# Kernel optimization log

Measured on AMD Instinct MI355X. Metric: run time of the kernel, lower is better.

The kernel has to match this reference:

```python
import jax, jax.numpy as jnp
import numpy as np

B, S, D, H = 2, 2048, 1024, 16
HD = D // H  # 64


def setup_inputs() -> dict:
    key = jax.random.key(0)
    k1, k2, k3, k4, k5, k6 = jax.random.split(key, 6)
    x = jax.random.normal(k1, (B, S, D), dtype=jnp.float32)
    # binary mask source (1.0 = masked-out position), multiplied by -1e9 inside
    mask = (jax.random.uniform(k2, (B, S, S), dtype=jnp.float32) < 0.1).astype(jnp.float32)
    lim = 1.0 / np.sqrt(D)
    Wqkv = jax.random.uniform(k3, (D, 3 * D), dtype=jnp.float32, minval=-lim, maxval=lim)
    bqkv = jax.random.uniform(k4, (3 * D,), dtype=jnp.float32, minval=-lim, maxval=lim)
    Wo = jax.random.uniform(k5, (D, D), dtype=jnp.float32, minval=-lim, maxval=lim)
    bo = jax.random.uniform(k6, (D,), dtype=jnp.float32, minval=-lim, maxval=lim)
    return {"x": x, "mask": mask, "Wqkv": Wqkv, "bqkv": bqkv, "Wo": Wo, "bo": bo}


def reference(x, mask, Wqkv, bqkv, Wo, bo):
    b, s, d = x.shape
    qkv = x @ Wqkv + bqkv                              # [B,S,3D]
    qkv = qkv.reshape(b, s, 3, H, HD).transpose(2, 0, 3, 1, 4)  # [3,B,H,S,HD]
    q, k, v = qkv[0], qkv[1], qkv[2]
    scale = 1.0 / jnp.sqrt(jnp.float32(HD))
    scores = jnp.einsum('bhqd,bhkd->bhqk', q, k) * scale
    scores = scores + mask[:, None, :, :] * (-1e9)     # broadcast over heads
    attn = jax.nn.softmax(scores, axis=-1)             # [B,H,S,S]
    values = jnp.einsum('bhqk,bhkd->bhqd', attn, v)    # [B,H,S,HD]
    # faithful to source: permute(1,0,2,3) then reshape(B,S,H*HD)
    values = values.transpose(1, 0, 2, 3).reshape(b, s, H * HD)
    return values @ Wo + bo
```

## Files before the change

### kernel.cpp

```cpp
#include <hip/hip_runtime.h>
#include <stdint.h>

#define BB 2
#define SS 2048
#define DD 1024
#define HH 16
#define HD 64
#define BH 32
#define BS 4096

typedef short bf16x8 __attribute__((ext_vector_type(8)));
typedef float f32x4 __attribute__((ext_vector_type(4)));

static __device__ __forceinline__ unsigned short f2bf(float f) {
    union { float f; unsigned int u; } x;
    x.f = f;
    unsigned int u = x.u;
    unsigned int r = u + 0x7FFFu + ((u >> 16) & 1u);
    return (unsigned short)(r >> 16);
}

static __device__ __forceinline__ void gld16(unsigned short* lds, const unsigned short* g) {
    __builtin_amdgcn_global_load_lds(
        (const __attribute__((address_space(1))) unsigned int*)g,
        (__attribute__((address_space(3))) unsigned int*)lds,
        16, 0, 0);
}

__global__ __launch_bounds__(256) void prep(
    const float* __restrict__ x, unsigned short* __restrict__ xb,
    const float* __restrict__ Wqkv, unsigned short* __restrict__ WqkvT,
    const float* __restrict__ Wo, unsigned short* __restrict__ WoT,
    const float* __restrict__ mask, unsigned int* __restrict__ mbitsT) {
    __shared__ float tile[32][33];
    int bid = blockIdx.x;
    int tid = threadIdx.x;
    if (bid < 4096) {
        int i = (bid * 256 + tid) * 4;
        float4 v = *(const float4*)(x + i);
        ushort4 o;
        o.x = f2bf(v.x); o.y = f2bf(v.y); o.z = f2bf(v.z); o.w = f2bf(v.w);
        *(ushort4*)(xb + i) = o;
    } else if (bid < 8192) {
        const float* W;
        unsigned short* WT;
        int N, t;
        if (bid < 7168) { W = Wqkv; WT = WqkvT; N = 3072; t = bid - 4096; }
        else            { W = Wo;   WT = WoT;   N = 1024; t = bid - 7168; }
        const int K = 1024;
        int nx = N >> 5;
        int n0 = (t % nx) * 32, k0 = (t / nx) * 32;
        int tx = tid & 31, ty = tid >> 5;
#pragma unroll
        for (int i = 0; i < 4; i++)
            tile[ty + i * 8][tx] = W[(size_t)(k0 + ty + i * 8) * N + n0 + tx];
        __syncthreads();
#pragma unroll
        for (int i = 0; i < 4; i++)
            WT[(size_t)(n0 + ty + i * 8) * K + k0 + tx] = f2bf(tile[tx][ty + i * 8]);
    } else {
        size_t i = (size_t)(bid - 8192) * 256 + tid;
        float v = mask[i];
        unsigned long long bal = __ballot(v != 0.0f);
        int lane = tid & 63;
        int kw = (int)((i & 2047) >> 5);
        int sq = (int)((i >> 11) & 2047);
        int b = (int)(i >> 22);
        if (lane == 0)
            mbitsT[((size_t)b * 64 + kw) * 2048 + sq] = (unsigned int)bal;
        else if (lane == 32)
            mbitsT[((size_t)b * 64 + kw) * 2048 + sq] = (unsigned int)(bal >> 32);
    }
}

__global__ __launch_bounds__(256) void qkv_gemm(
    const unsigned short* __restrict__ xb,
    const unsigned short* __restrict__ WqkvT,
    const float* __restrict__ bqkv,
    unsigned short* __restrict__ q_ws,
    unsigned short* __restrict__ k_ws,
    unsigned short* __restrict__ vB) {
    __shared__ unsigned short ldsA[4096], ldsB[4096];
    int gx = blockIdx.x;
    int tid = threadIdx.x;
    int m0 = (gx / 24) * 128, n0 = (gx % 24) * 128;
    int w = tid >> 6, lane = tid & 63, quad = lane >> 4, l15 = lane & 15;

    int r = tid >> 2, p = tid & 3;
    int c = (p - (r >> 1)) & 3;
    const unsigned short* gA0 = xb + (size_t)(m0 + r) * 1024 + c * 8;
    const unsigned short* gA1 = gA0 + (size_t)64 * 1024;
    const unsigned short* gB0 = WqkvT + (size_t)(n0 + r) * 1024 + c * 8;
    const unsigned short* gB1 = gB0 + (size_t)64 * 1024;
    unsigned short* lA0 = ldsA + w * 512;
    unsigned short* lA1 = ldsA + 2048 + w * 512;
    unsigned short* lB0 = ldsB + w * 512;
    unsigned short* lB1 = ldsB + 2048 + w * 512;

    int wm = w >> 1, wn = w & 1;
    int posq = ((quad + (l15 >> 1)) & 3) * 8;
    int aoff = (wm * 64 + l15) * 32 + posq;
    int boff = (wn * 64 + l15) * 32 + posq;

    f32x4 acc[4][4] = {};
    for (int k0 = 0; k0 < 1024; k0 += 32) {
        __syncthreads();
        gld16(lA0, gA0 + k0);
        gld16(lA1, gA1 + k0);
        gld16(lB0, gB0 + k0);
        gld16(lB1, gB1 + k0);
        __syncthreads();
        bf16x8 af[4], bfr[4];
#pragma unroll
        for (int i = 0; i < 4; i++) {
            af[i]  = *(const bf16x8*)(ldsA + aoff + i * 512);
            bfr[i] = *(const bf16x8*)(ldsB + boff + i * 512);
        }
#pragma unroll
        for (int i = 0; i < 4; i++)
#pragma unroll
            for (int j = 0; j < 4; j++)
                acc[i][j] = __builtin_amdgcn_mfma_f32_16x16x32_bf16(af[i], bfr[j], acc[i][j], 0, 0, 0);
    }

    int t = n0 >> 10;
    int ncol0 = n0 + wn * 64;
    int hh = (ncol0 >> 6) & 15;
    int Rb = m0 + wm * 64 + quad * 4;

    if (t == 2) {
        int rowbase = m0 + wm * 64;
        int b = rowbase >> 11;
        int kt = (rowbase >> 6) & 31;
        int bh = b * 16 + hh;
#pragma unroll
        for (int j = 0; j < 4; j++) {
            int hd = j * 16 + l15;
            float bias = bqkv[ncol0 + hd];
#pragma unroll
            for (int i = 0; i < 4; i++) {
                unsigned short* dst = vB +
                    (((((size_t)bh * 32 + kt) * 2 + (i >> 1)) * 4 + quad) * 64 + hd) * 8 + (i & 1) * 4;
                ushort4 pk;
                pk.x = f2bf(acc[i][j][0] + bias);
                pk.y = f2bf(acc[i][j][1] + bias);
                pk.z = f2bf(acc[i][j][2] + bias);
                pk.w = f2bf(acc[i][j][3] + bias);
                *(ushort4*)dst = pk;
            }
        }
    } else {
        unsigned short* dst = (t == 0) ? q_ws : k_ws;
#pragma unroll
        for (int j = 0; j < 4; j++) {
            int hd = j * 16 + l15;
            float bias = bqkv[ncol0 + hd];
#pragma unroll
            for (int i = 0; i < 4; i++) {
                int row = Rb + i * 16;
                int b = row >> 11, s = row & 2047;
                int bh = b * 16 + hh;
#pragma unroll
                for (int rr = 0; rr < 4; rr++)
                    dst[((size_t)(bh * 2048 + s + rr)) * 64 + hd] = f2bf(acc[i][j][rr] + bias);
            }
        }
    }
}

__global__ __launch_bounds__(256) void out_gemm(
    const unsigned short* __restrict__ Amat,
    const unsigned short* __restrict__ WoT,
    const float* __restrict__ bo,
    float* __restrict__ out) {
    __shared__ unsigned short ldsA[4096], ldsB[2048];
    int gx = blockIdx.x;
    int m0 = (gx / 16) * 128, n0 = (gx % 16) * 64;
    int tid = threadIdx.x;
    int w = tid >> 6, lane = tid & 63, quad = lane >> 4, l15 = lane & 15;

    int r = tid >> 2, p = tid & 3;
    int c = (p - (r >> 1)) & 3;
    const unsigned short* gA0 = Amat + (size_t)(m0 + r) * 1024 + c * 8;
    const unsigned short* gA1 = gA0 + (size_t)64 * 1024;
    const unsigned short* gB0 = WoT + (size_t)(n0 + r) * 1024 + c * 8;
    unsigned short* lA0 = ldsA + w * 512;
    unsigned short* lA1 = ldsA + 2048 + w * 512;
    unsigned short* lB0 = ldsB + w * 512;

    int wm = w >> 1, wn = w & 1;
    int posq = ((quad + (l15 >> 1)) & 3) * 8;
    int aoff = (wm * 64 + l15) * 32 + posq;
    int boff = (wn * 32 + l15) * 32 + posq;

    f32x4 acc[4][2] = {};
    for (int k0 = 0; k0 < 1024; k0 += 32) {
        __syncthreads();
        gld16(lA0, gA0 + k0);
        gld16(lA1, gA1 + k0);
        gld16(lB0, gB0 + k0);
        __syncthreads();
        bf16x8 af[4], bfr[2];
#pragma unroll
        for (int i = 0; i < 4; i++) af[i] = *(const bf16x8*)(ldsA + aoff + i * 512);
#pragma unroll
        for (int j = 0; j < 2; j++) bfr[j] = *(const bf16x8*)(ldsB + boff + j * 512);
#pragma unroll
        for (int i = 0; i < 4; i++)
#pragma unroll
            for (int j = 0; j < 2; j++)
                acc[i][j] = __builtin_amdgcn_mfma_f32_16x16x32_bf16(af[i], bfr[j], acc[i][j], 0, 0, 0);
    }
    int ncol0 = n0 + wn * 32;
    int Rb = m0 + wm * 64 + quad * 4;
#pragma unroll
    for (int j = 0; j < 2; j++) {
        int col = ncol0 + j * 16 + l15;
        float bias = bo[col];
#pragma unroll
        for (int i = 0; i < 4; i++) {
            int row = Rb + i * 16;
#pragma unroll
            for (int rr = 0; rr < 4; rr++)
                out[(size_t)(row + rr) * 1024 + col] = acc[i][j][rr] + bias;
        }
    }
}

__global__ __launch_bounds__(256) void attn(
    const unsigned short* __restrict__ q_ws,
    const unsigned short* __restrict__ k_ws,
    const unsigned short* __restrict__ vB,
    const unsigned int* __restrict__ mbitsT,
    unsigned short* __restrict__ o_ws) {
    __shared__ unsigned short ldsK[8192];
    __shared__ unsigned short ldsV[8192];

    int tid = threadIdx.x;
    int w = tid >> 6, lane = tid & 63, quad = lane >> 4, l15 = lane & 15;
    int bxr = blockIdx.x;
    int bx = ((bxr & 7) << 7) | (bxr >> 3);
    int bh = bx >> 5, qt = bx & 31;
    int b = bh >> 4, h = bh & 15;

    int q = qt * 64 + w * 16 + l15;
    const unsigned short* qptr = q_ws + ((size_t)(bh * 2048 + q)) * 64 + quad * 8;
    bf16x8 qf0 = *(const bf16x8*)(qptr);
    bf16x8 qf1 = *(const bf16x8*)(qptr + 32);

    const float c2 = 0.125f * 1.44269504089f;
    const float Cs = c2 * 8388608.0f;
    const float Ds = (127.0f - 16.0f) * 8388608.0f;

    const unsigned int* mb = mbitsT + (size_t)b * 64 * 2048 + q;
    const unsigned short* kbase = k_ws + (size_t)bh * 2048 * 64;
    const unsigned short* vbb = vB + (size_t)bh * 32 * 4096;

    int srow = (lane >> 3);
    int spos = lane & 7;
    unsigned short* dK0 = ldsK + w * 1024 + lane * 8;
    unsigned short* dV0 = ldsV + w * 1024 + lane * 8;
    int r0 = w * 16 + srow;
    int r1 = r0 + 8;
    int g0 = spos ^ (r0 & 7);
    int g1 = spos ^ (r1 & 7);
    const unsigned short* kS0n = kbase + (size_t)r0 * 64 + g0 * 8;
    const unsigned short* kS1n = kbase + (size_t)r1 * 64 + g1 * 8;
    const unsigned short* vSn  = vbb + (size_t)w * 1024 + lane * 8;
    const unsigned int* mbn = mb;

    f32x4 oacc[4] = {};
    f32x4 lacc = {};
    bf16x8 onesA;
#pragma unroll
    for (int j = 0; j < 8; j++) onesA[j] = (short)0x3F80;

    int sw = (l15 & 7);
    int q4 = quad * 4;

    gld16(dK0, kS0n);
    gld16(dK0 + 512, kS1n);
    gld16(dV0, vSn);
    gld16(dV0 + 512, vSn + 512);
    kS0n += 4096; kS1n += 4096; vSn += 4096;
    unsigned int mw0 = mbn[0];
    unsigned int mw1 = mbn[2048];
    mbn += 4096;
    __syncthreads();

    unsigned int nw0, nw1;

#define ATTN_BODY(KT, CO)                                                          \
    {                                                                              \
        nw0 = 0; nw1 = 0;                                                          \
        if ((KT) < 31) {                 \
            gld16(dK0 + ((CO) ^ 4096), kS0n);                                      \
            gld16(dK0 + ((CO) ^ 4096) + 512, kS1n);                                \
            gld16(dV0 + ((CO) ^ 4096), vSn);                                       \
            gld16(dV0 + ((CO) ^ 4096) + 512, vSn + 512);                           \
            kS0n += 4096; kS1n += 4096; vSn += 4096;                               \
            nw0 = mbn[0]; nw1 = mbn[2048]; mbn += 4096;                            \
        }                                                                          \
        f32x4 sacc[4];                                                             \
        __builtin_amdgcn_s_setprio(1);                                             \
        _Pragma("unroll")                                                          \
        for (int nt = 0; nt < 4; nt++) {                                           \
            const unsigned short* kr = ldsK + (CO) + (nt * 16 + l15) * 64;         \
            bf16x8 kf0, kf1;                                                       \
            __builtin_memcpy(&kf0, kr + (quad ^ sw) * 8, 16);                      \
            __builtin_memcpy(&kf1, kr + ((quad + 4) ^ sw) * 8, 16);                \
            f32x4 z = {};                                                          \
            z = __builtin_amdgcn_mfma_f32_16x16x32_bf16(kf0, qf0, z, 0, 0, 0);     \
            z = __builtin_amdgcn_mfma_f32_16x16x32_bf16(kf1, qf1, z, 0, 0, 0);     \
            sacc[nt] = z;                                                          \
        }                                                                          \
        __builtin_amdgcn_s_setprio(0);                                             \
        unsigned int s0 = mw0 >> q4;                                               \
        unsigned int s1 = mw1 >> q4;                                               \
        unsigned int dw[4][2];                                                     \
        _Pragma("unroll")                                                          \
        for (int nt = 0; nt < 4; nt++) {                                           \
            unsigned int sel = (nt & 2) ? s1 : s0;                                 \
            unsigned int u[4];                                                     \
            _Pragma("unroll")                                                      \
            for (int rr = 0; rr < 4; rr++) {                                       \
                float y = __builtin_fmaf(sacc[nt][rr], Cs, Ds);                    \
                if ((sel >> ((nt & 1) * 16 + rr)) & 1u) y = 0.f;                   \
                u[rr] = (unsigned int)(int)y;                                      \
            }                                                                      \
            dw[nt][0] = __builtin_amdgcn_perm(u[1], u[0], 0x07060302u);            \
            dw[nt][1] = __builtin_amdgcn_perm(u[3], u[2], 0x07060302u);            \
        }                                                                          \
        __builtin_amdgcn_s_setprio(1);                                             \
        _Pragma("unroll")                                                          \
        for (int ks2 = 0; ks2 < 2; ks2++) {                                        \
            union { bf16x8 v; unsigned int d[4]; } bfr;                            \
            bfr.d[0] = dw[2 * ks2][0];                                             \
            bfr.d[1] = dw[2 * ks2][1];                                             \
            bfr.d[2] = dw[2 * ks2 + 1][0];                                         \
            bfr.d[3] = dw[2 * ks2 + 1][1];                                         \
            _Pragma("unroll")                                                      \
            for (int nb = 0; nb < 4; nb++) {                                       \
                bf16x8 vf;                                                         \
                __builtin_memcpy(&vf,                                              \
                    ldsV + (CO) + ((ks2 * 4 + quad) * 64 + nb * 16 + l15) * 8, 16);\
                oacc[nb] = __builtin_amdgcn_mfma_f32_16x16x32_bf16(vf, bfr.v,      \
                                                                   oacc[nb], 0, 0, 0); \
            }                                                                      \
            lacc = __builtin_amdgcn_mfma_f32_16x16x32_bf16(onesA, bfr.v, lacc,     \
                                                           0, 0, 0);               \
        }                                                                          \
        __builtin_amdgcn_s_setprio(0);                                             \
        __syncthreads();               \
        mw0 = nw0; mw1 = nw1;                                                      \
    }

    for (int kt = 0; kt < 32; kt += 2) {
        ATTN_BODY(kt, 0);
        ATTN_BODY(kt + 1, 4096);
    }
#undef ATTN_BODY

    float linv = 1.0f / lacc[0];
    unsigned short* base = o_ws + ((size_t)((h * 2 + b) * 2048 + q)) * 64;
#pragma unroll
    for (int nb = 0; nb < 4; nb++) {
        ushort4 pk;
        pk.x = f2bf(oacc[nb][0] * linv);
        pk.y = f2bf(oacc[nb][1] * linv);
        pk.z = f2bf(oacc[nb][2] * linv);
        pk.w = f2bf(oacc[nb][3] * linv);
        *(ushort4*)(base + nb * 16 + quad * 4) = pk;
    }
}


extern "C" void kernel_launch(void* const* d_in, const int* in_sizes, int n_in,
                              void* d_out, int out_size, void* d_ws, size_t ws_size,
                              hipStream_t stream) {
    const float* x    = (const float*)d_in[0];
    const float* mask = (const float*)d_in[1];
    const float* Wqkv = (const float*)d_in[2];
    const float* bqkv = (const float*)d_in[3];
    const float* Wo   = (const float*)d_in[4];
    const float* bo   = (const float*)d_in[5];
    float* out = (float*)d_out;

    char* ws = (char*)d_ws;
    unsigned short* xb    = (unsigned short*)(ws);
    unsigned short* WqkvT = (unsigned short*)(ws + ((size_t)8 << 20));
    unsigned short* WoT   = (unsigned short*)(ws + ((size_t)14 << 20));
    unsigned short* q_ws  = (unsigned short*)(ws + ((size_t)16 << 20));
    unsigned short* k_ws  = (unsigned short*)(ws + ((size_t)24 << 20));
    unsigned short* vB    = (unsigned short*)(ws + ((size_t)32 << 20));
    unsigned short* o_ws  = (unsigned short*)(ws + ((size_t)40 << 20));
    unsigned int*   mbits = (unsigned int*)(ws + ((size_t)48 << 20));

    prep<<<8192 + 32768, 256, 0, stream>>>(x, xb, Wqkv, WqkvT, Wo, WoT, mask, mbits);
    qkv_gemm<<<768, 256, 0, stream>>>(xb, WqkvT, bqkv, q_ws, k_ws, vB);
    attn<<<1024, 256, 0, stream>>>(q_ws, k_ws, vB, mbits, o_ws);
    out_gemm<<<512, 256, 0, stream>>>(o_ws, WoT, bo, out);
}
```

Measured before the change: 232.3 us.

## Split attention waves across key halves with two query tiles each, reduce via LDS

Each of the four waves in the attention block now handles 32 queries (two 16-query tiles) over half of each 64-key tile, instead of 16 queries over the full key tile. Every K fragment read from LDS and every V fragment is now reused for two MFMA query tiles, roughly halving LDS fragment reads per MFMA. The two key-half partial output and row-sum accumulators are merged through LDS at the end. This costs an extra barrier and reduction, plus more accumulator registers per thread.

```diff
diff --git a/kernel.cpp b/kernel.cpp
--- a/kernel.cpp
+++ b/kernel.cpp
@@ -238,21 +238,25 @@
 
     int tid = threadIdx.x;
     int w = tid >> 6, lane = tid & 63, quad = lane >> 4, l15 = lane & 15;
+    int wk = w >> 1, wq = w & 1;
     int bxr = blockIdx.x;
     int bx = ((bxr & 7) << 7) | (bxr >> 3);
     int bh = bx >> 5, qt = bx & 31;
     int b = bh >> 4, h = bh & 15;
 
-    int q = qt * 64 + w * 16 + l15;
-    const unsigned short* qptr = q_ws + ((size_t)(bh * 2048 + q)) * 64 + quad * 8;
-    bf16x8 qf0 = *(const bf16x8*)(qptr);
-    bf16x8 qf1 = *(const bf16x8*)(qptr + 32);
+    int qA = qt * 64 + wq * 32 + l15;
+    const unsigned short* qptrA = q_ws + ((size_t)(bh * 2048 + qA)) * 64 + quad * 8;
+    bf16x8 qfA0 = *(const bf16x8*)(qptrA);
+    bf16x8 qfA1 = *(const bf16x8*)(qptrA + 32);
+    const unsigned short* qptrB = qptrA + 16 * 64;
+    bf16x8 qfB0 = *(const bf16x8*)(qptrB);
+    bf16x8 qfB1 = *(const bf16x8*)(qptrB + 32);
 
     const float c2 = 0.125f * 1.44269504089f;
     const float Cs = c2 * 8388608.0f;
     const float Ds = (127.0f - 16.0f) * 8388608.0f;
 
-    const unsigned int* mb = mbitsT + (size_t)b * 64 * 2048 + q;
+    const unsigned int* mbn = mbitsT + (size_t)b * 64 * 2048 + qA + (size_t)wk * 2048;
     const unsigned short* kbase = k_ws + (size_t)bh * 2048 * 64;
     const unsigned short* vbb = vB + (size_t)bh * 32 * 4096;
 
@@ -267,92 +271,99 @@
     const unsigned short* kS0n = kbase + (size_t)r0 * 64 + g0 * 8;
     const unsigned short* kS1n = kbase + (size_t)r1 * 64 + g1 * 8;
     const unsigned short* vSn  = vbb + (size_t)w * 1024 + lane * 8;
-    const unsigned int* mbn = mb;
-
-    f32x4 oacc[4] = {};
-    f32x4 lacc = {};
+
+    f32x4 oaccA[4] = {}, oaccB[4] = {};
+    f32x4 laccA = {}, laccB = {};
     bf16x8 onesA;
 #pragma unroll
     for (int j = 0; j < 8; j++) onesA[j] = (short)0x3F80;
 
     int sw = (l15 & 7);
     int q4 = quad * 4;
+    int krow = wk * 32;
+    int voff = (wk * 4 + quad) * 64;
 
     gld16(dK0, kS0n);
     gld16(dK0 + 512, kS1n);
     gld16(dV0, vSn);
     gld16(dV0 + 512, vSn + 512);
     kS0n += 4096; kS1n += 4096; vSn += 4096;
-    unsigned int mw0 = mbn[0];
-    unsigned int mw1 = mbn[2048];
+    unsigned int mwA = mbn[0];
+    unsigned int mwB = mbn[16];
     mbn += 4096;
     __syncthreads();
 
-    unsigned int nw0, nw1;
+    unsigned int nwA, nwB;
 
 #define ATTN_BODY(KT, CO)                                                          \
     {                                                                              \
-        nw0 = 0; nw1 = 0;                                                          \
+        nwA = 0; nwB = 0;                                                          \
         if ((KT) < 31) {                 \
             gld16(dK0 + ((CO) ^ 4096), kS0n);                                      \
             gld16(dK0 + ((CO) ^ 4096) + 512, kS1n);                                \
             gld16(dV0 + ((CO) ^ 4096), vSn);                                       \
             gld16(dV0 + ((CO) ^ 4096) + 512, vSn + 512);                           \
             kS0n += 4096; kS1n += 4096; vSn += 4096;                               \
-            nw0 = mbn[0]; nw1 = mbn[2048]; mbn += 4096;                            \
+            nwA = mbn[0]; nwB = mbn[16]; mbn += 4096;                              \
         }                                                                          \
-        f32x4 sacc[4];                                                             \
+        f32x4 saccA[2], saccB[2];                                                  \
         __builtin_amdgcn_s_setprio(1);                                             \
         _Pragma("unroll")                                                          \
-        for (int nt = 0; nt < 4; nt++) {                                           \
-            const unsigned short* kr = ldsK + (CO) + (nt * 16 + l15) * 64;         \
+        for (int i = 0; i < 2; i++) {                                              \
+            const unsigned short* kr = ldsK + (CO) + (krow + i * 16 + l15) * 64;   \
             bf16x8 kf0, kf1;                                                       \
             __builtin_memcpy(&kf0, kr + (quad ^ sw) * 8, 16);                      \
             __builtin_memcpy(&kf1, kr + ((quad + 4) ^ sw) * 8, 16);                \
-            f32x4 z = {};                                                          \
-            z = __builtin_amdgcn_mfma_f32_16x16x32_bf16(kf0, qf0, z, 0, 0, 0);     \
-            z = __builtin_amdgcn_mfma_f32_16x16x32_bf16(kf1, qf1, z, 0, 0, 0);     \
-            sacc[nt] = z;                                                          \
+            f32x4 zA = {};                                                         \
+            zA = __builtin_amdgcn_mfma_f32_16x16x32_bf16(kf0, qfA0, zA, 0, 0, 0);  \
+            zA = __builtin_amdgcn_mfma_f32_16x16x32_bf16(kf1, qfA1, zA, 0, 0, 0);  \
+            saccA[i] = zA;                                                         \
+            f32x4 zB = {};                                                         \
+            zB = __builtin_amdgcn_mfma_f32_16x16x32_bf16(kf0, qfB0, zB, 0, 0, 0);  \
+            zB = __builtin_amdgcn_mfma_f32_16x16x32_bf16(kf1, qfB1, zB, 0, 0, 0);  \
+            saccB[i] = zB;                                                         \
         }                                                                          \
         __builtin_amdgcn_s_setprio(0);                                             \
-        unsigned int s0 = mw0 >> q4;                                               \
-        unsigned int s1 = mw1 >> q4;                                               \
-        unsigned int dw[4][2];                                                     \
+        unsigned int sA = mwA >> q4;                                               \
+        unsigned int sB = mwB >> q4;                                               \
+        unsigned int dwA[2][2], dwB[2][2];                                         \
         _Pragma("unroll")                                                          \
-        for (int nt = 0; nt < 4; nt++) {                                           \
-            unsigned int sel = (nt & 2) ? s1 : s0;                                 \
-            unsigned int u[4];                                                     \
+        for (int i = 0; i < 2; i++) {                                              \
+            unsigned int uA[4], uB[4];                                             \
             _Pragma("unroll")                                                      \
             for (int rr = 0; rr < 4; rr++) {                                       \
-                float y = __builtin_fmaf(sacc[nt][rr], Cs, Ds);                    \
-                if ((sel >> ((nt & 1) * 16 + rr)) & 1u) y = 0.f;                   \
-                u[rr] = (unsigned int)(int)y;                                      \
+                float yA = __builtin_fmaf(saccA[i][rr], Cs, Ds);                   \
+                if ((sA >> (i * 16 + rr)) & 1u) yA = 0.f;                          \
+                uA[rr] = (unsigned int)(int)yA;                                    \
+                float yB = __builtin_fmaf(saccB[i][rr], Cs, Ds);                   \
+                if ((sB >> (i * 16 + rr)) & 1u) yB = 0.f;                          \
+                uB[rr] = (unsigned int)(int)yB;                                    \
             }                                                                      \
-            dw[nt][0] = __builtin_amdgcn_perm(u[1], u[0], 0x07060302u);            \
-            dw[nt][1] = __builtin_amdgcn_perm(u[3], u[2], 0x07060302u);            \
+            dwA[i][0] = __builtin_amdgcn_perm(uA[1], uA[0], 0x07060302u);          \
+            dwA[i][1] = __builtin_amdgcn_perm(uA[3], uA[2], 0x07060302u);          \
+            dwB[i][0] = __builtin_amdgcn_perm(uB[1], uB[0], 0x07060302u);          \
+            dwB[i][1] = __builtin_amdgcn_perm(uB[3], uB[2], 0x07060302u);          \
         }                                                                          \
+        union { bf16x8 v; unsigned int d[4]; } bA, bB;                             \
+        bA.d[0] = dwA[0][0]; bA.d[1] = dwA[0][1];                                  \
+        bA.d[2] = dwA[1][0]; bA.d[3] = dwA[1][1];                                  \
+        bB.d[0] = dwB[0][0]; bB.d[1] = dwB[0][1];                                  \
+        bB.d[2] = dwB[1][0]; bB.d[3] = dwB[1][1];                                  \
         __builtin_amdgcn_s_setprio(1);                                             \
         _Pragma("unroll")                                                          \
-        for (int ks2 = 0; ks2 < 2; ks2++) {                                        \
-            union { bf16x8 v; unsigned int d[4]; } bfr;                            \
-            bfr.d[0] = dw[2 * ks2][0];                                             \
-            bfr.d[1] = dw[2 * ks2][1];                                             \
-            bfr.d[2] = dw[2 * ks2 + 1][0];                                         \
-            bfr.d[3] = dw[2 * ks2 + 1][1];                                         \
-            _Pragma("unroll")                                                      \
-            for (int nb = 0; nb < 4; nb++) {                                       \
-                bf16x8 vf;                                                         \
-                __builtin_memcpy(&vf,                                              \
-                    ldsV + (CO) + ((ks2 * 4 + quad) * 64 + nb * 16 + l15) * 8, 16);\
-                oacc[nb] = __builtin_amdgcn_mfma_f32_16x16x32_bf16(vf, bfr.v,      \
-                                                                   oacc[nb], 0, 0, 0); \
-            }                                                                      \
-            lacc = __builtin_amdgcn_mfma_f32_16x16x32_bf16(onesA, bfr.v, lacc,     \
-                                                           0, 0, 0);               \
+        for (int nb = 0; nb < 4; nb++) {                                           \
+            bf16x8 vf;                                                             \
+            __builtin_memcpy(&vf, ldsV + (CO) + (voff + nb * 16 + l15) * 8, 16);   \
+            oaccA[nb] = __builtin_amdgcn_mfma_f32_16x16x32_bf16(vf, bA.v,          \
+                                                                oaccA[nb], 0, 0, 0);   \
+            oaccB[nb] = __builtin_amdgcn_mfma_f32_16x16x32_bf16(vf, bB.v,          \
+                                                                oaccB[nb], 0, 0, 0);   \
         }                                                                          \
+        laccA = __builtin_amdgcn_mfma_f32_16x16x32_bf16(onesA, bA.v, laccA, 0, 0, 0);  \
+        laccB = __builtin_amdgcn_mfma_f32_16x16x32_bf16(onesA, bB.v, laccB, 0, 0, 0);  \
         __builtin_amdgcn_s_setprio(0);                                             \
         __syncthreads();               \
-        mw0 = nw0; mw1 = nw1;                                                      \
+        mwA = nwA; mwB = nwB;                                                      \
     }
 
     for (int kt = 0; kt < 32; kt += 2) {
@@ -361,16 +372,44 @@
     }
 #undef ATTN_BODY
 
-    float linv = 1.0f / lacc[0];
-    unsigned short* base = o_ws + ((size_t)((h * 2 + b) * 2048 + q)) * 64;
-#pragma unroll
-    for (int nb = 0; nb < 4; nb++) {
-        ushort4 pk;
-        pk.x = f2bf(oacc[nb][0] * linv);
-        pk.y = f2bf(oacc[nb][1] * linv);
-        pk.z = f2bf(oacc[nb][2] * linv);
-        pk.w = f2bf(oacc[nb][3] * linv);
-        *(ushort4*)(base + nb * 16 + quad * 4) = pk;
+    float* SF = (float*)ldsK;
+    float* SL = (float*)ldsV;
+    if (wk == 1) {
+        int off = (wq * 64 + lane) * 32;
+#pragma unroll
+        for (int nb = 0; nb < 4; nb++) {
+            *(f32x4*)(SF + off + nb * 4)      = oaccA[nb];
+            *(f32x4*)(SF + off + 16 + nb * 4) = oaccB[nb];
+        }
+        SL[wq * 128 + lane]      = laccA[0];
+        SL[wq * 128 + 64 + lane] = laccB[0];
+    }
+    __syncthreads();
+    if (wk == 0) {
+        int off = (wq * 64 + lane) * 32;
+        float lA = laccA[0] + SL[wq * 128 + lane];
+        float lB = laccB[0] + SL[wq * 128 + 64 + lane];
+        float linvA = 1.0f / lA;
+        float linvB = 1.0f / lB;
+        unsigned short* baseA = o_ws + ((size_t)((h * 2 + b) * 2048 + qA)) * 64;
+        unsigned short* baseB = baseA + 16 * 64;
+#pragma unroll
+        for (int nb = 0; nb < 4; nb++) {
+            f32x4 pA = *(f32x4*)(SF + off + nb * 4);
+            f32x4 pB = *(f32x4*)(SF + off + 16 + nb * 4);
+            ushort4 pkA;
+            pkA.x = f2bf((oaccA[nb][0] + pA[0]) * linvA);
+            pkA.y = f2bf((oaccA[nb][1] + pA[1]) * linvA);
+            pkA.z = f2bf((oaccA[nb][2] + pA[2]) * linvA);
+            pkA.w = f2bf((oaccA[nb][3] + pA[3]) * linvA);
+            *(ushort4*)(baseA + nb * 16 + quad * 4) = pkA;
+            ushort4 pkB;
+            pkB.x = f2bf((oaccB[nb][0] + pB[0]) * linvB);
+            pkB.y = f2bf((oaccB[nb][1] + pB[1]) * linvB);
+            pkB.z = f2bf((oaccB[nb][2] + pB[2]) * linvB);
+            pkB.w = f2bf((oaccB[nb][3] + pB[3]) * linvB);
+            *(ushort4*)(baseB + nb * 16 + quad * 4) = pkB;
+        }
     }
 }
 
```

Result: slower. 247.8 us (+6.7%).

## Vectorize mask bit-packing per row and remap GEMM blocks for XCD locality

Applied to the files above, without the earlier changes.

The mask packing path now has each thread read 32 consecutive floats with float4 loads and build a 32-bit word directly. This replaces the per-element ballot, so the prep grid drops from about 41K blocks to 9216. Both GEMM kernels remap block indices so that blocks scheduled on the same XCD share the same rows of A, aiming for better L2 reuse across the chiplets. The per-thread loads are now strided across lanes, which may coalesce less well than before.

```diff
diff --git a/kernel.cpp b/kernel.cpp
--- a/kernel.cpp
+++ b/kernel.cpp
@@ -59,17 +59,20 @@
         for (int i = 0; i < 4; i++)
             WT[(size_t)(n0 + ty + i * 8) * K + k0 + tx] = f2bf(tile[tx][ty + i * 8]);
     } else {
-        size_t i = (size_t)(bid - 8192) * 256 + tid;
-        float v = mask[i];
-        unsigned long long bal = __ballot(v != 0.0f);
-        int lane = tid & 63;
-        int kw = (int)((i & 2047) >> 5);
-        int sq = (int)((i >> 11) & 2047);
-        int b = (int)(i >> 22);
-        if (lane == 0)
-            mbitsT[((size_t)b * 64 + kw) * 2048 + sq] = (unsigned int)bal;
-        else if (lane == 32)
-            mbitsT[((size_t)b * 64 + kw) * 2048 + sq] = (unsigned int)(bal >> 32);
+        int w = tid >> 6, lane = tid & 63;
+        int row = (bid - 8192) * 4 + w;
+        int b = row >> 11, sq = row & 2047;
+        const float* mrow = mask + ((size_t)b * 2048 + sq) * 2048 + lane * 32;
+        unsigned int wbits = 0;
+#pragma unroll
+        for (int c = 0; c < 8; c++) {
+            float4 v = *(const float4*)(mrow + c * 4);
+            wbits |= (v.x != 0.0f ? 1u : 0u) << (c * 4);
+            wbits |= (v.y != 0.0f ? 2u : 0u) << (c * 4);
+            wbits |= (v.z != 0.0f ? 4u : 0u) << (c * 4);
+            wbits |= (v.w != 0.0f ? 8u : 0u) << (c * 4);
+        }
+        mbitsT[((size_t)b * 64 + lane) * 2048 + sq] = wbits;
     }
 }
 
@@ -81,9 +84,11 @@
     unsigned short* __restrict__ k_ws,
     unsigned short* __restrict__ vB) {
     __shared__ unsigned short ldsA[4096], ldsB[4096];
-    int gx = blockIdx.x;
+    int gxr = blockIdx.x;
     int tid = threadIdx.x;
-    int m0 = (gx / 24) * 128, n0 = (gx % 24) * 128;
+    int xcd = gxr & 7, lidx = gxr >> 3;
+    int m0 = (xcd * 4 + (lidx & 3)) * 128;
+    int n0 = (lidx >> 2) * 128;
     int w = tid >> 6, lane = tid & 63, quad = lane >> 4, l15 = lane & 15;
 
     int r = tid >> 2, p = tid & 3;
@@ -174,8 +179,10 @@
     const float* __restrict__ bo,
     float* __restrict__ out) {
     __shared__ unsigned short ldsA[4096], ldsB[2048];
-    int gx = blockIdx.x;
-    int m0 = (gx / 16) * 128, n0 = (gx % 16) * 64;
+    int gxr = blockIdx.x;
+    int xcd = gxr & 7, lidx = gxr >> 3;
+    int m0 = (xcd * 4 + (lidx & 3)) * 128;
+    int n0 = (lidx >> 2) * 64;
     int tid = threadIdx.x;
     int w = tid >> 6, lane = tid & 63, quad = lane >> 4, l15 = lane & 15;
 
@@ -396,7 +403,7 @@
     unsigned short* o_ws  = (unsigned short*)(ws + ((size_t)40 << 20));
     unsigned int*   mbits = (unsigned int*)(ws + ((size_t)48 << 20));
 
-    prep<<<8192 + 32768, 256, 0, stream>>>(x, xb, Wqkv, WqkvT, Wo, WoT, mask, mbits);
+    prep<<<9216, 256, 0, stream>>>(x, xb, Wqkv, WqkvT, Wo, WoT, mask, mbits);
     qkv_gemm<<<768, 256, 0, stream>>>(xb, WqkvT, bqkv, q_ws, k_ws, vB);
     attn<<<1024, 256, 0, stream>>>(q_ws, k_ws, vB, mbits, o_ws);
     out_gemm<<<512, 256, 0, stream>>>(o_ws, WoT, bo, out);
```

Result: faster. 225.8 us (-2.8%).
